# Kernel optimization log

Hardware: AMD Instinct MI355X
Metric: run time of the kernel (lower is better)

The kernel has to match this reference:

```python
import jax, jax.numpy as jnp
import numpy as np

K = 40        # nearest neighbors
BN_EPS = 1e-5  # nn.BatchNorm1d default eps


def _bn(x, g, b):
    # training-mode BatchNorm1d: batch mean, biased variance
    mu = x.mean(0)
    var = x.var(0)
    return g * (x - mu) / jnp.sqrt(var + BN_EPS) + b


def setup_inputs() -> dict:
    key = jax.random.key(0)
    ks = jax.random.split(key, 16)
    N, Cin, D, S, P = 8192, 16, 32, 3, 32

    def w(k, i, o):
        return jax.random.normal(k, (i, o), jnp.float32) * (1.0 / np.sqrt(i))

    return {
        "x": jax.random.normal(ks[0], (N, Cin), jnp.float32),
        "original_coords": jax.random.normal(ks[1], (N, 3), jnp.float32),
        "batch": jnp.zeros((N,), jnp.int32),
        "step_count": 0,
        "num_layer": 1,
        # pre_gravnet MLP
        "pre_w1": w(ks[2], Cin, D), "pre_b1": jnp.zeros((D,), jnp.float32),
        "pre_w2": w(ks[3], D, D), "pre_b2": jnp.zeros((D,), jnp.float32),
        "bn1_g": jnp.ones((D,), jnp.float32), "bn1_b": jnp.zeros((D,), jnp.float32),
        # GravNetConv projections
        "lin_s_w": w(ks[4], D, S),
        "lin_h_w": w(ks[5], D, P), "lin_h_b": jnp.zeros((P,), jnp.float32),
        "lin_w": w(ks[6], D + 2 * P, D), "lin_b": jnp.zeros((D,), jnp.float32),
        # post_gravnet MLP (in = out_channels + space_dims + d_shape = 32+3+32)
        "post_w1": w(ks[7], D + S + D, D), "post_b1": jnp.zeros((D,), jnp.float32),
        "post_w2": w(ks[8], D, D), "post_b2": jnp.zeros((D,), jnp.float32),
        "bn2_g": jnp.ones((D,), jnp.float32), "bn2_b": jnp.zeros((D,), jnp.float32),
    }


def reference(x, original_coords, batch, step_count, num_layer,
              pre_w1, pre_b1, pre_w2, pre_b2, bn1_g, bn1_b,
              lin_s_w, lin_h_w, lin_h_b, lin_w, lin_b,
              post_w1, post_b1, post_w2, post_b2, bn2_g, bn2_b):
    N = x.shape[0]

    # pre_gravnet MLP + batchnorm
    h = jax.nn.elu(x @ pre_w1 + pre_b1)
    h = jax.nn.elu(h @ pre_w2 + pre_b2)
    x_in = _bn(h, bn1_g, bn1_b)

    # GravNetConv projections
    h_l = x_in @ lin_h_w + lin_h_b          # [N, P] propagated features
    s_l = x_in @ lin_s_w                    # [N, S] learned coordinate space

    # kNN graph in s-space (self loops excluded)
    sq = jnp.sum(s_l * s_l, axis=1)
    d2 = sq[:, None] + sq[None, :] - 2.0 * (s_l @ s_l.T)   # [N, N]
    d2 = jnp.maximum(d2, 0.0)
    d2 = jnp.where(jnp.eye(N, dtype=bool), jnp.inf, d2)
    _, idx = jax.lax.top_k(-d2, K)           # [N, K] neighbor indices

    # per-edge squared distance (NOTE: propagate uses the SQUARED distance,
    # faithful to the source where edge_weight is never re-bound to sqrt)
    edge_sq = jnp.take_along_axis(d2, idx, axis=1)    # [N, K]
    dist = jnp.sqrt(edge_sq + 1e-6)                   # [N, K]

    # DGL-side reductions at dst = edge_index[1] = neighbor index
    dst = idx.reshape(-1)
    distf = dist.reshape(-1)
    indeg = jax.ops.segment_sum(jnp.ones_like(distf), dst, num_segments=N)
    sum_d = jax.ops.segment_sum(distf, dst, num_segments=N)
    avdist = jnp.where(indeg > 0, sum_d / jnp.maximum(indeg, 1.0), 0.0)
    loss_regularizing_neig = 0.01 * jnp.mean(jnp.square(avdist - 0.5))

    norm_d = distf / (sum_d + 1e-4)[dst]              # EdgeWeightNorm('right')
    # faithful to source bug: '_edge_w_gndist' is set to the NORMALIZED dist,
    # and apply_edges multiplies by the RAW '_edge_w'
    degs2 = jax.ops.segment_sum(norm_d, dst, num_segments=N) + 1e-4
    gn_final = distf / degs2[dst]
    loss_llregulariser = 0.1 * jnp.mean(jnp.square(norm_d - gn_final))

    # message passing: msg = h_l[neighbor] * squared_dist, mean+max over the
    # K neighbors of each source node (regular fan-in -> dense reduce)
    msgs = h_l[idx] * edge_sq[..., None]              # [N, K, P]
    agg = jnp.concatenate([msgs.mean(1), msgs.max(1)], axis=-1)  # [N, 2P]
    xgn = jnp.concatenate([agg, x_in], axis=-1) @ lin_w + lin_b   # [N, 32]

    # post_gravnet MLP + batchnorm
    cat = jnp.concatenate([xgn, s_l, x_in], axis=1)   # [N, 67]
    o = jax.nn.elu(cat @ post_w1 + post_b1)
    o = jax.nn.elu(o @ post_w2 + post_b2)
    out = _bn(o, bn2_g, bn2_b)
    return (out, loss_regularizing_neig, loss_llregulariser)
```

## Files before the change

### kernel.cpp

```cpp
#include <hip/hip_runtime.h>
#include <math.h>

#define NPTS 8192
#define KNN 40
#define DD 32
#define CIN 16
#define RPB 8
#define QT 2048
#define NQTR 4
#define KQPB 16
#define CAP 96

#define OFF_H      0u
#define OFF_XIN    262144u
#define OFF_HL     524288u
#define OFF_SL     786432u
#define OFF_ESQ    819200u
#define OFF_O      1146880u
#define OFF_IDX    1409024u
#define OFF_SUMD   1736704u
#define OFF_INDEG  1744896u
#define OFF_STATS  1753088u
#define ZERO_FLOATS (8192u + 8192u + 130u * 32u)

#define ST(i) stats[(i) * 32]

__device__ __forceinline__ float elu_f(float x) { return x > 0.f ? x : (expf(x) - 1.f); }

__device__ __forceinline__ float grp_sum32(float v) {
#pragma unroll
    for (int m = 1; m < 32; m <<= 1) v += __shfl_xor(v, m);
    return v;
}

__device__ __forceinline__ float rfl(float v) {
    return __int_as_float(__builtin_amdgcn_readfirstlane(__float_as_int(v)));
}

__device__ __forceinline__ unsigned fkey(float x) {
    unsigned b = __float_as_uint(x);
    return b ^ ((unsigned)((int)b >> 31) | 0x80000000u);
}
__device__ __forceinline__ float kinv(unsigned k) {
    unsigned b = (k & 0x80000000u) ? (k ^ 0x80000000u) : ~k;
    return __uint_as_float(b);
}

__device__ __forceinline__ unsigned bisect_kth(unsigned u0, unsigned u1, int kth) {
    unsigned lo = 0u, hi = 0xFFFFFFFFu;
    while (lo < hi) {
        unsigned mid = lo + ((hi - lo) >> 1);
        int cnt = __popcll(__ballot(u0 <= mid)) + __popcll(__ballot(u1 <= mid));
        if (cnt >= kth) hi = mid; else lo = mid + 1;
    }
    return hi;
}

__global__ __launch_bounds__(256) void k_pre(const float* __restrict__ x,
    const float* __restrict__ w1, const float* __restrict__ b1,
    const float* __restrict__ w2, const float* __restrict__ b2,
    float* __restrict__ h, float* __restrict__ stats)
{
    __shared__ float sw1[CIN * DD], sw2[DD * DD], sb1[DD], sb2[DD];
    __shared__ float bufx[RPB][20], buft[RPB][36];
    __shared__ float sstat[2 * DD];
    int tid = threadIdx.x;
    for (int t = tid; t < CIN * DD; t += 256) sw1[t] = w1[t];
    for (int t = tid; t < DD * DD; t += 256) sw2[t] = w2[t];
    if (tid < DD) { sb1[tid] = b1[tid]; sb2[tid] = b2[tid]; }
    if (tid < 2 * DD) sstat[tid] = 0.f;

    int r = tid >> 5, ch = tid & 31;
    int g = blockIdx.x * RPB + r;
    if (ch < CIN) bufx[r][ch] = x[(size_t)g * CIN + ch];
    __syncthreads();

    float acc = sb1[ch];
#pragma unroll
    for (int k4 = 0; k4 < CIN; k4 += 4) {
        float4 v = *(const float4*)&bufx[r][k4];
        acc = fmaf(v.x, sw1[(k4 + 0) * DD + ch], acc);
        acc = fmaf(v.y, sw1[(k4 + 1) * DD + ch], acc);
        acc = fmaf(v.z, sw1[(k4 + 2) * DD + ch], acc);
        acc = fmaf(v.w, sw1[(k4 + 3) * DD + ch], acc);
    }
    acc = elu_f(acc);
    buft[r][ch] = acc;
    __syncthreads();

    float o = sb2[ch];
#pragma unroll
    for (int k4 = 0; k4 < DD; k4 += 4) {
        float4 v = *(const float4*)&buft[r][k4];
        o = fmaf(v.x, sw2[(k4 + 0) * DD + ch], o);
        o = fmaf(v.y, sw2[(k4 + 1) * DD + ch], o);
        o = fmaf(v.z, sw2[(k4 + 2) * DD + ch], o);
        o = fmaf(v.w, sw2[(k4 + 3) * DD + ch], o);
    }
    o = elu_f(o);
    h[(size_t)g * DD + ch] = o;

    float s = o + __shfl_xor(o, 32);
    float q = o * o;
    q += __shfl_xor(q, 32);
    if ((tid & 32) == 0) { atomicAdd(&sstat[ch], s); atomicAdd(&sstat[DD + ch], q); }
    __syncthreads();
    if (tid < 2 * DD) atomicAdd(&ST(tid), sstat[tid]);
}

__global__ __launch_bounds__(256) void k_proj(const float* __restrict__ h,
    const float* __restrict__ stats,
    const float* __restrict__ g1, const float* __restrict__ b1g,
    const float* __restrict__ hw, const float* __restrict__ hb,
    const float* __restrict__ sw,
    float* __restrict__ xin, float* __restrict__ hl, float4* __restrict__ sl4)
{
    __shared__ float shw[DD * DD], ssw[DD * 3], sa[DD], sbp[DD], shb[DD];
    __shared__ float rrow[RPB][36];
    int tid = threadIdx.x;
    for (int t = tid; t < DD * DD; t += 256) shw[t] = hw[t];
    if (tid < DD * 3) ssw[tid] = sw[tid];
    if (tid < DD) {
        float mean = ST(tid) * (1.f / NPTS);
        float var = ST(32 + tid) * (1.f / NPTS) - mean * mean;
        float a = g1[tid] * rsqrtf(var + 1e-5f);
        sa[tid] = a;
        sbp[tid] = b1g[tid] - a * mean;
        shb[tid] = hb[tid];
    }
    __syncthreads();

    int r = tid >> 5, ch = tid & 31;
    int g = blockIdx.x * RPB + r;

    float v = fmaf(sa[ch], h[(size_t)g * DD + ch], sbp[ch]);
    xin[(size_t)g * DD + ch] = v;
    rrow[r][ch] = v;

    float p0 = v * ssw[ch * 3 + 0];
    float p1 = v * ssw[ch * 3 + 1];
    float p2 = v * ssw[ch * 3 + 2];
    p0 = grp_sum32(p0); p1 = grp_sum32(p1); p2 = grp_sum32(p2);
    if (ch == 0) sl4[g] = make_float4(p0, p1, p2, 0.5f * (p0 * p0 + p1 * p1 + p2 * p2));
    __syncthreads();

    float o = shb[ch];
#pragma unroll
    for (int k4 = 0; k4 < DD; k4 += 4) {
        float4 vv = *(const float4*)&rrow[r][k4];
        o = fmaf(vv.x, shw[(k4 + 0) * DD + ch], o);
        o = fmaf(vv.y, shw[(k4 + 1) * DD + ch], o);
        o = fmaf(vv.z, shw[(k4 + 2) * DD + ch], o);
        o = fmaf(vv.w, shw[(k4 + 3) * DD + ch], o);
    }
    hl[(size_t)g * DD + ch] = o;
}

__device__ __forceinline__ void select_emit(const float2* bufq, int C, int qidx,
    float qw, int lane, int* __restrict__ idxo, float* __restrict__ esq,
    float* __restrict__ sumd, float* __restrict__ indeg)
{
    float e0 = INFINITY, e1 = INFINITY;
    int j0 = -1, j1 = -1;
    if (lane < C) { float2 t = bufq[lane]; e0 = t.x; j0 = __float_as_int(t.y); }
    if (lane + 64 < C) { float2 t = bufq[lane + 64]; e1 = t.x; j1 = __float_as_int(t.y); }
    if (j0 == qidx) e0 = INFINITY;
    if (j1 == qidx) e1 = INFINITY;
    unsigned u0 = fkey(e0), u1 = fkey(e1);
    unsigned thr = bisect_kth(u0, u1, KNN);
    unsigned long long ltm = (1ull << lane) - 1;
    unsigned long long mlt0 = __ballot(u0 < thr), mlt1 = __ballot(u1 < thr);
    unsigned long long meq0 = __ballot(u0 == thr), meq1 = __ballot(u1 == thr);
    int nlt = __popcll(mlt0) + __popcll(mlt1);
    int need = KNN - nlt;
    int rb = qidx * KNN;

    int pos = -1;
    if (u0 < thr) pos = __popcll(mlt0 & ltm);
    else if (u0 == thr) { int rk = __popcll(meq0 & ltm); if (rk < need) pos = nlt + rk; }
    if (pos >= 0) {
        float d2 = fmaxf(2.f * (e0 + qw), 0.f);
        idxo[rb + pos] = j0; esq[rb + pos] = d2;
        float dist = sqrtf(d2 + 1e-6f);
        atomicAdd(&sumd[j0], dist); atomicAdd(&indeg[j0], 1.f);
    }
    pos = -1;
    if (u1 < thr) pos = __popcll(mlt0) + __popcll(mlt1 & ltm);
    else if (u1 == thr) {
        int rk = __popcll(meq0) + __popcll(meq1 & ltm);
        if (rk < need) pos = nlt + rk;
    }
    if (pos >= 0) {
        float d2 = fmaxf(2.f * (e1 + qw), 0.f);
        idxo[rb + pos] = j1; esq[rb + pos] = d2;
        float dist = sqrtf(d2 + 1e-6f);
        atomicAdd(&sumd[j1], dist); atomicAdd(&indeg[j1], 1.f);
    }
}

typedef __attribute__((address_space(1))) const unsigned glds_src_t;
typedef __attribute__((address_space(3))) unsigned glds_dst_t;

__global__ __launch_bounds__(512, 4) void k_knn(const float4* __restrict__ sl4,
    int* __restrict__ idxo, float* __restrict__ esq,
    float* __restrict__ sumd, float* __restrict__ indeg)
{
    __shared__ float4 tile[2][QT];
    __shared__ float2 cand[KQPB][CAP];
    int tid = threadIdx.x, lane = tid & 63, w = tid >> 6;
    int qbase = blockIdx.x * KQPB;
    int qai = qbase + 2 * w, qbi = qai + 1;
    float4 qa4 = sl4[qai], qb4 = sl4[qbi];
    float qax = rfl(qa4.x), qay = rfl(qa4.y), qaz = rfl(qa4.z);
    float qbx = rfl(qb4.x), qby = rfl(qb4.y), qbz = rfl(qb4.z);

#define STAGE(qt, b) { \
    _Pragma("unroll") \
    for (int c = 0; c < 4; ++c) { \
        int off = w * 256 + c * 64; \
        __builtin_amdgcn_global_load_lds( \
            (glds_src_t*)(sl4 + (qt) * QT + off + lane), \
            (glds_dst_t*)&tile[b][off], 16, 0, 0); \
    } }

#define EDQ(p, ex, ey, ez) fmaf(-(ex), (p).x, fmaf(-(ey), (p).y, fmaf(-(ez), (p).z, (p).w)))

    float m0a = INFINITY, m1a = INFINITY, m0b = INFINITY, m1b = INFINITY;
    STAGE(0, 0)
    __syncthreads();
    for (int t = 0; t < NQTR; ++t) {
        if (t + 1 < NQTR) STAGE(t + 1, (t + 1) & 1)
        const float4* tp = tile[t & 1];
#pragma unroll 4
        for (int i = 0; i < QT / 64; ++i) {
            float4 p = tp[i * 64 + lane];
            float ea = EDQ(p, qax, qay, qaz);
            float eb = EDQ(p, qbx, qby, qbz);
            float lo = fminf(ea, m0a), hi = fmaxf(ea, m0a);
            m0a = lo; m1a = fminf(m1a, hi);
            lo = fminf(eb, m0b); hi = fmaxf(eb, m0b);
            m0b = lo; m1b = fminf(m1b, hi);
        }
        __syncthreads();
    }
    float thra = kinv(bisect_kth(fkey(m0a), fkey(m1a), KNN + 1));
    float thrb = kinv(bisect_kth(fkey(m0b), fkey(m1b), KNN + 1));

    unsigned long long ltm = (1ull << lane) - 1;
    int ca = 0, cb = 0;
    float2* bufa = cand[2 * w];
    float2* bufb = cand[2 * w + 1];

#define COLL(e, thrv, cnt, brow, jj) { \
        unsigned long long mm = __ballot((e) <= (thrv)); \
        if (mm) { \
            if ((e) <= (thrv)) { \
                int pos = cnt + __popcll(mm & ltm); \
                if (pos < CAP) brow[pos] = make_float2((e), __int_as_float(jj)); \
            } \
            cnt += __popcll(mm); \
        } }

    STAGE(0, 0)
    __syncthreads();
    for (int t = 0; t < NQTR; ++t) {
        if (t + 1 < NQTR) STAGE(t + 1, (t + 1) & 1)
        const float4* tp = tile[t & 1];
        int tb = t * QT;
#pragma unroll 4
        for (int i = 0; i < QT / 64; ++i) {
            float4 p = tp[i * 64 + lane];
            int jj = tb + i * 64 + lane;
            float ea = EDQ(p, qax, qay, qaz);
            float eb = EDQ(p, qbx, qby, qbz);
            COLL(ea, thra, ca, bufa, jj)
            COLL(eb, thrb, cb, bufb, jj)
        }
        __syncthreads();
    }

    select_emit(bufa, ca < CAP ? ca : CAP, qai, rfl(qa4.w), lane, idxo, esq, sumd, indeg);
    select_emit(bufb, cb < CAP ? cb : CAP, qbi, rfl(qb4.w), lane, idxo, esq, sumd, indeg);
}

__global__ __launch_bounds__(256) void k_agg(
    const int* __restrict__ idx, const float* __restrict__ esq,
    const float* __restrict__ hl, const float* __restrict__ xin,
    const float4* __restrict__ sl4,
    const float* __restrict__ sumd, const float* __restrict__ indeg,
    const float* __restrict__ lw, const float* __restrict__ lb,
    const float* __restrict__ pw1, const float* __restrict__ pb1,
    const float* __restrict__ pw2, const float* __restrict__ pb2,
    float* __restrict__ o, float* __restrict__ stats)
{
    __shared__ float slw[96 * DD], spw1[67 * DD], spw2[DD * DD];
    __shared__ float slb[DD], spb1[DD], spb2[DD];
    __shared__ float rbuf[RPB][100];
    __shared__ float rb2[RPB][68];
    __shared__ float sstat[2 * DD];
    __shared__ float sl1, sl2;
    int tid = threadIdx.x;
    for (int t = tid; t < 96 * DD; t += 256) slw[t] = lw[t];
    for (int t = tid; t < 67 * DD; t += 256) spw1[t] = pw1[t];
    for (int t = tid; t < DD * DD; t += 256) spw2[t] = pw2[t];
    if (tid < DD) { slb[tid] = lb[tid]; spb1[tid] = pb1[tid]; spb2[tid] = pb2[tid]; }
    if (tid < 2 * DD) sstat[tid] = 0.f;
    if (tid == 254) sl1 = 0.f;
    if (tid == 255) sl2 = 0.f;

    int r = tid >> 5, ch = tid & 31;
    int g = blockIdx.x * RPB + r;
    int rb = g * KNN;

    float sv = 0.f, mv = -INFINITY;
#pragma unroll 8
    for (int k = 0; k < KNN; ++k) {
        int j = idx[rb + k];
        float w = esq[rb + k];
        float m = hl[(size_t)j * DD + ch] * w;
        sv += m;
        mv = fmaxf(mv, m);
    }
    rbuf[r][ch] = sv * (1.f / KNN);
    rbuf[r][32 + ch] = mv;
    rbuf[r][64 + ch] = xin[(size_t)g * DD + ch];
    if (ch == 0) { float4 s = sl4[g]; rbuf[r][96] = s.x; rbuf[r][97] = s.y; rbuf[r][98] = s.z; }
    __syncthreads();

    float l2 = 0.f;
    {
        int j = idx[rb + ch];
        float w = esq[rb + ch];
        float dist = sqrtf(w + 1e-6f);
        float sd = sumd[j];
        float r1 = 1.f / (sd + 1e-4f);
        float dg = sd * r1 + 1e-4f;
        float df = dist * r1 - dist / dg;
        l2 = df * df;
        if (ch < KNN - 32) {
            j = idx[rb + 32 + ch];
            w = esq[rb + 32 + ch];
            dist = sqrtf(w + 1e-6f);
            sd = sumd[j];
            r1 = 1.f / (sd + 1e-4f);
            dg = sd * r1 + 1e-4f;
            df = dist * r1 - dist / dg;
            l2 += df * df;
        }
    }
    l2 = grp_sum32(l2);
    if (ch == 0) {
        float id = indeg[g], sdg = sumd[g];
        float av = id > 0.f ? sdg / fmaxf(id, 1.f) : 0.f;
        float dd = av - 0.5f;
        atomicAdd(&sl2, l2);
        atomicAdd(&sl1, dd * dd);
    }

    float acc = slb[ch];
#pragma unroll
    for (int k4 = 0; k4 < 96; k4 += 4) {
        float4 v = *(const float4*)&rbuf[r][k4];
        acc = fmaf(v.x, slw[(k4 + 0) * DD + ch], acc);
        acc = fmaf(v.y, slw[(k4 + 1) * DD + ch], acc);
        acc = fmaf(v.z, slw[(k4 + 2) * DD + ch], acc);
        acc = fmaf(v.w, slw[(k4 + 3) * DD + ch], acc);
    }
    rb2[r][ch] = acc;
    __syncthreads();

    acc = spb1[ch];
#pragma unroll
    for (int k4 = 0; k4 < DD; k4 += 4) {
        float4 v = *(const float4*)&rb2[r][k4];
        acc = fmaf(v.x, spw1[(k4 + 0) * DD + ch], acc);
        acc = fmaf(v.y, spw1[(k4 + 1) * DD + ch], acc);
        acc = fmaf(v.z, spw1[(k4 + 2) * DD + ch], acc);
        acc = fmaf(v.w, spw1[(k4 + 3) * DD + ch], acc);
    }
#pragma unroll
    for (int s2 = 0; s2 < 3; ++s2)
        acc = fmaf(rbuf[r][96 + s2], spw1[(32 + s2) * DD + ch], acc);
#pragma unroll
    for (int k4 = 0; k4 < DD; k4 += 4) {
        float4 v = *(const float4*)&rbuf[r][64 + k4];
        acc = fmaf(v.x, spw1[(35 + k4 + 0) * DD + ch], acc);
        acc = fmaf(v.y, spw1[(35 + k4 + 1) * DD + ch], acc);
        acc = fmaf(v.z, spw1[(35 + k4 + 2) * DD + ch], acc);
        acc = fmaf(v.w, spw1[(35 + k4 + 3) * DD + ch], acc);
    }
    acc = elu_f(acc);
    rb2[r][32 + ch] = acc;
    __syncthreads();

    acc = spb2[ch];
#pragma unroll
    for (int k4 = 0; k4 < DD; k4 += 4) {
        float4 v = *(const float4*)&rb2[r][32 + k4];
        acc = fmaf(v.x, spw2[(k4 + 0) * DD + ch], acc);
        acc = fmaf(v.y, spw2[(k4 + 1) * DD + ch], acc);
        acc = fmaf(v.z, spw2[(k4 + 2) * DD + ch], acc);
        acc = fmaf(v.w, spw2[(k4 + 3) * DD + ch], acc);
    }
    acc = elu_f(acc);
    o[(size_t)g * DD + ch] = acc;

    float s = acc + __shfl_xor(acc, 32);
    float q = acc * acc;
    q += __shfl_xor(q, 32);
    if ((tid & 32) == 0) { atomicAdd(&sstat[ch], s); atomicAdd(&sstat[DD + ch], q); }
    __syncthreads();
    if (tid < 2 * DD) atomicAdd(&ST(64 + tid), sstat[tid]);
    if (tid == 0) { atomicAdd(&ST(128), sl1); atomicAdd(&ST(129), sl2); }
}

__global__ __launch_bounds__(256) void k_out(const float* __restrict__ o,
    const float* __restrict__ stats, const float* __restrict__ g,
    const float* __restrict__ b, float* __restrict__ dout)
{
    __shared__ float sa[DD], sb[DD];
    int tid = threadIdx.x;
    if (tid < DD) {
        float mean = ST(64 + tid) * (1.f / NPTS);
        float var = ST(96 + tid) * (1.f / NPTS) - mean * mean;
        float a = g[tid] * rsqrtf(var + 1e-5f);
        sa[tid] = a;
        sb[tid] = b[tid] - a * mean;
    }
    __syncthreads();

    int t = blockIdx.x * 256 + tid;
    float4 v = ((const float4*)o)[t];
    int cbase = (t * 4) & (DD - 1);
    float4 rr;
    rr.x = fmaf(sa[cbase + 0], v.x, sb[cbase + 0]);
    rr.y = fmaf(sa[cbase + 1], v.y, sb[cbase + 1]);
    rr.z = fmaf(sa[cbase + 2], v.z, sb[cbase + 2]);
    rr.w = fmaf(sa[cbase + 3], v.w, sb[cbase + 3]);
    ((float4*)dout)[t] = rr;

    if (blockIdx.x == 0) {
        if (tid == DD)     dout[NPTS * DD]     = 0.01f * ST(128) * (1.f / NPTS);
        if (tid == DD + 1) dout[NPTS * DD + 1] = 0.1f  * ST(129) * (1.f / ((float)NPTS * KNN));
    }
}

extern "C" void kernel_launch(void* const* d_in, const int* in_sizes, int n_in,
                              void* d_out, int out_size, void* d_ws, size_t ws_size,
                              hipStream_t stream)
{
    (void)in_sizes; (void)n_in; (void)out_size; (void)ws_size;
    const float* x      = (const float*)d_in[0];
    const float* pre_w1 = (const float*)d_in[5];
    const float* pre_b1 = (const float*)d_in[6];
    const float* pre_w2 = (const float*)d_in[7];
    const float* pre_b2 = (const float*)d_in[8];
    const float* bn1_g  = (const float*)d_in[9];
    const float* bn1_b  = (const float*)d_in[10];
    const float* lin_s_w = (const float*)d_in[11];
    const float* lin_h_w = (const float*)d_in[12];
    const float* lin_h_b = (const float*)d_in[13];
    const float* lin_w   = (const float*)d_in[14];
    const float* lin_b   = (const float*)d_in[15];
    const float* post_w1 = (const float*)d_in[16];
    const float* post_b1 = (const float*)d_in[17];
    const float* post_w2 = (const float*)d_in[18];
    const float* post_b2 = (const float*)d_in[19];
    const float* bn2_g   = (const float*)d_in[20];
    const float* bn2_b   = (const float*)d_in[21];

    float* W = (float*)d_ws;
    float* h     = W + OFF_H;
    float* xin   = W + OFF_XIN;
    float* hl    = W + OFF_HL;
    float4* sl4  = (float4*)(W + OFF_SL);
    float* esq   = W + OFF_ESQ;
    float* o     = W + OFF_O;
    int*   idx   = (int*)(W + OFF_IDX);
    float* sumd  = W + OFF_SUMD;
    float* indeg = W + OFF_INDEG;
    float* stats = W + OFF_STATS;
    float* dout  = (float*)d_out;

    hipMemsetAsync(W + OFF_SUMD, 0, ZERO_FLOATS * sizeof(float), stream);

    k_pre<<<NPTS / RPB, 256, 0, stream>>>(x, pre_w1, pre_b1, pre_w2, pre_b2, h, stats);
    k_proj<<<NPTS / RPB, 256, 0, stream>>>(h, stats, bn1_g, bn1_b,
                                           lin_h_w, lin_h_b, lin_s_w, xin, hl, sl4);
    k_knn<<<NPTS / KQPB, 512, 0, stream>>>(sl4, idx, esq, sumd, indeg);
    k_agg<<<NPTS / RPB, 256, 0, stream>>>(idx, esq, hl, xin, sl4, sumd, indeg,
                                          lin_w, lin_b, post_w1, post_b1, post_w2, post_b2,
                                          o, stats);
    k_out<<<NPTS * DD / 1024, 256, 0, stream>>>(o, stats, bn2_g, bn2_b, dout);
}
```

Baseline: 120.6 us.

## Stage all points into LDS once per 1024-thread kNN block

The kNN kernel now loads the whole 8192-point coordinate array (128 KB) into shared memory once per block, instead of double-buffering 2048-point tiles across two passes. Blocks grow to 1024 threads handling 32 queries, so each staged copy serves twice as many queries and the per-tile syncs go away. This uses much more LDS per block (128 KB plus candidate buffers), which limits how many blocks fit on a CU. It also drops the overlap between loading and compute, and the launch-bounds hint of 4 blocks of 1024 cannot be met.

```diff
diff --git a/kernel.cpp b/kernel.cpp
--- a/kernel.cpp
+++ b/kernel.cpp
@@ -6,9 +6,7 @@
 #define DD 32
 #define CIN 16
 #define RPB 8
-#define QT 2048
-#define NQTR 4
-#define KQPB 16
+#define KQPB 32
 #define CAP 96
 
 #define OFF_H      0u
@@ -201,11 +199,13 @@
 typedef __attribute__((address_space(1))) const unsigned glds_src_t;
 typedef __attribute__((address_space(3))) unsigned glds_dst_t;
 
-__global__ __launch_bounds__(512, 4) void k_knn(const float4* __restrict__ sl4,
+#define EDQ(p, ex, ey, ez) fmaf(-(ex), (p).x, fmaf(-(ey), (p).y, fmaf(-(ez), (p).z, (p).w)))
+
+__global__ __launch_bounds__(1024, 4) void k_knn(const float4* __restrict__ sl4,
     int* __restrict__ idxo, float* __restrict__ esq,
     float* __restrict__ sumd, float* __restrict__ indeg)
 {
-    __shared__ float4 tile[2][QT];
+    __shared__ float4 tile[NPTS];
     __shared__ float2 cand[KQPB][CAP];
     int tid = threadIdx.x, lane = tid & 63, w = tid >> 6;
     int qbase = blockIdx.x * KQPB;
@@ -214,34 +214,25 @@
     float qax = rfl(qa4.x), qay = rfl(qa4.y), qaz = rfl(qa4.z);
     float qbx = rfl(qb4.x), qby = rfl(qb4.y), qbz = rfl(qb4.z);
 
-#define STAGE(qt, b) { \
-    _Pragma("unroll") \
-    for (int c = 0; c < 4; ++c) { \
-        int off = w * 256 + c * 64; \
-        __builtin_amdgcn_global_load_lds( \
-            (glds_src_t*)(sl4 + (qt) * QT + off + lane), \
-            (glds_dst_t*)&tile[b][off], 16, 0, 0); \
-    } }
-
-#define EDQ(p, ex, ey, ez) fmaf(-(ex), (p).x, fmaf(-(ey), (p).y, fmaf(-(ez), (p).z, (p).w)))
+#pragma unroll
+    for (int k = 0; k < NPTS / 1024; ++k) {
+        int off = k * 1024 + w * 64;
+        __builtin_amdgcn_global_load_lds(
+            (glds_src_t*)(sl4 + off + lane),
+            (glds_dst_t*)&tile[off], 16, 0, 0);
+    }
+    __syncthreads();
 
     float m0a = INFINITY, m1a = INFINITY, m0b = INFINITY, m1b = INFINITY;
-    STAGE(0, 0)
-    __syncthreads();
-    for (int t = 0; t < NQTR; ++t) {
-        if (t + 1 < NQTR) STAGE(t + 1, (t + 1) & 1)
-        const float4* tp = tile[t & 1];
 #pragma unroll 4
-        for (int i = 0; i < QT / 64; ++i) {
-            float4 p = tp[i * 64 + lane];
-            float ea = EDQ(p, qax, qay, qaz);
-            float eb = EDQ(p, qbx, qby, qbz);
-            float lo = fminf(ea, m0a), hi = fmaxf(ea, m0a);
-            m0a = lo; m1a = fminf(m1a, hi);
-            lo = fminf(eb, m0b); hi = fmaxf(eb, m0b);
-            m0b = lo; m1b = fminf(m1b, hi);
-        }
-        __syncthreads();
+    for (int i = 0; i < NPTS / 64; ++i) {
+        float4 p = tile[i * 64 + lane];
+        float ea = EDQ(p, qax, qay, qaz);
+        float eb = EDQ(p, qbx, qby, qbz);
+        float lo = fminf(ea, m0a), hi = fmaxf(ea, m0a);
+        m0a = lo; m1a = fminf(m1a, hi);
+        lo = fminf(eb, m0b); hi = fmaxf(eb, m0b);
+        m0b = lo; m1b = fminf(m1b, hi);
     }
     float thra = kinv(bisect_kth(fkey(m0a), fkey(m1a), KNN + 1));
     float thrb = kinv(bisect_kth(fkey(m0b), fkey(m1b), KNN + 1));
@@ -261,22 +252,14 @@
             cnt += __popcll(mm); \
         } }
 
-    STAGE(0, 0)
-    __syncthreads();
-    for (int t = 0; t < NQTR; ++t) {
-        if (t + 1 < NQTR) STAGE(t + 1, (t + 1) & 1)
-        const float4* tp = tile[t & 1];
-        int tb = t * QT;
 #pragma unroll 4
-        for (int i = 0; i < QT / 64; ++i) {
-            float4 p = tp[i * 64 + lane];
-            int jj = tb + i * 64 + lane;
-            float ea = EDQ(p, qax, qay, qaz);
-            float eb = EDQ(p, qbx, qby, qbz);
-            COLL(ea, thra, ca, bufa, jj)
-            COLL(eb, thrb, cb, bufb, jj)
-        }
-        __syncthreads();
+    for (int i = 0; i < NPTS / 64; ++i) {
+        float4 p = tile[i * 64 + lane];
+        int jj = i * 64 + lane;
+        float ea = EDQ(p, qax, qay, qaz);
+        float eb = EDQ(p, qbx, qby, qbz);
+        COLL(ea, thra, ca, bufa, jj)
+        COLL(eb, thrb, cb, bufb, jj)
     }
 
     select_emit(bufa, ca < CAP ? ca : CAP, qai, rfl(qa4.w), lane, idxo, esq, sumd, indeg);
@@ -487,7 +470,7 @@
     k_pre<<<NPTS / RPB, 256, 0, stream>>>(x, pre_w1, pre_b1, pre_w2, pre_b2, h, stats);
     k_proj<<<NPTS / RPB, 256, 0, stream>>>(h, stats, bn1_g, bn1_b,
                                            lin_h_w, lin_h_b, lin_s_w, xin, hl, sl4);
-    k_knn<<<NPTS / KQPB, 512, 0, stream>>>(sl4, idx, esq, sumd, indeg);
+    k_knn<<<NPTS / KQPB, 1024, 0, stream>>>(sl4, idx, esq, sumd, indeg);
     k_agg<<<NPTS / RPB, 256, 0, stream>>>(idx, esq, hl, xin, sl4, sumd, indeg,
                                           lin_w, lin_b, post_w1, post_b1, post_w2, post_b2,
                                           o, stats);
```

New measurement: 114.7 us, median of 2. 1.05x faster.
